# Optimization experiments

Hardware: AMD Instinct MI355X
Metric: run time of the kernel (lower is better)

## Reference

```python
import jax, jax.numpy as jnp
import numpy as np

B, H, L, D = 16, 8, 512, 64
TEMPERATURE = 8.0  # sqrt(d_k)
MASK_SENTINEL = -10000.0
BIG_NEG = 1e9


def setup_inputs() -> dict:
    key = jax.random.key(0)
    kq, kk, kv, km = jax.random.split(key, 4)
    q = jax.random.normal(kq, (B * H, L, D), dtype=jnp.float32)
    k = jax.random.normal(kk, (B * H, L, D), dtype=jnp.float32)
    v = jax.random.normal(kv, (B * H, L, D), dtype=jnp.float32)
    mask = jnp.where(jax.random.bernoulli(km, 0.1, (B, L)), MASK_SENTINEL, 0.0).astype(jnp.float32)
    return {"q": q, "k": k, "v": v, "mask": mask, "n_head": H}


def reference(q, k, v, mask, n_head):
    # attn: [B*H, L, L]
    attn = jnp.einsum("bid,bjd->bij", q, k) / TEMPERATURE
    # masked_fill(mask == -10000, 1e9); other values subtracted as-is
    m = jnp.where(mask == MASK_SENTINEL, BIG_NEG, mask)          # [B, L]
    m_bh = jnp.repeat(m, n_head, axis=0)                          # [B*H, L], matches reshape(B*H, ...)
    # row mask (mask.unsqueeze(-1).repeat) and its transpose (column mask)
    attn = attn - m_bh[:, :, None] - m_bh[:, None, :]
    attn = jax.nn.softmax(attn, axis=2)
    # dropout in eval mode (identity) for the deterministic reference
    output = jnp.einsum("bij,bjd->bid", attn, v)
    return output, attn
```

## Files before the change

kernel.cpp:

```cpp
#include <hip/hip_runtime.h>
#include <stdint.h>

#define Ln 512
#define Dn 64
#define BHn 128
#define AOFF ((size_t)BHn*Ln*Dn)

typedef __attribute__((ext_vector_type(8))) short short8;
typedef __attribute__((ext_vector_type(4))) float f32x4;
typedef __attribute__((ext_vector_type(4))) unsigned int u32x4;
typedef __attribute__((ext_vector_type(2))) unsigned int u32x2;

__device__ __forceinline__ uint16_t f2bf(float f){
  uint32_t x = __float_as_uint(f);
  return (uint16_t)((x + 0x7FFFu + ((x>>16)&1u)) >> 16);
}
__device__ __forceinline__ float bf2f(uint16_t u){ return __uint_as_float(((uint32_t)u)<<16); }
__device__ __forceinline__ uint32_t pack2(float a, float b){
  return (uint32_t)f2bf(a) | ((uint32_t)f2bf(b)<<16);
}
__device__ __forceinline__ void gld16(const uint16_t* g, uint16_t* l){
  __builtin_amdgcn_global_load_lds(
      (const __attribute__((address_space(1))) void*)g,
      (__attribute__((address_space(3))) void*)l, 16, 0, 0);
}

extern "C" __global__ __launch_bounds__(256)
void attn_prep(const float* __restrict__ kg, const float* __restrict__ vg,
               uint16_t* __restrict__ khw, uint16_t* __restrict__ klw,
               uint16_t* __restrict__ vtw)
{
  const int t  = threadIdx.x;
  const int c  = blockIdx.x;
  const int bh = blockIdx.y;
  const size_t base = (size_t)bh*(Ln*Dn);
  const size_t wsb  = ((size_t)bh<<15) + ((size_t)c<<13);

  {
    const int sj  = t>>1, skh = t&1;
    const float* kr = kg + base + (size_t)(c*128 + sj)*Dn + skh*32;
    const int sx = (sj&7)<<3;
    #pragma unroll
    for (int w2=0; w2<4; ++w2){
      f32x4 x0 = *(const f32x4*)(kr + w2*8);
      f32x4 x1 = *(const f32x4*)(kr + w2*8 + 4);
      uint32_t hw[4], lw[4];
      #pragma unroll
      for (int pi=0; pi<4; ++pi){
        float a0 = (pi<2) ? x0[pi*2]   : x1[(pi-2)*2];
        float a1 = (pi<2) ? x0[pi*2+1] : x1[(pi-2)*2+1];
        uint16_t h0 = f2bf(a0), h1 = f2bf(a1);
        hw[pi] = (uint32_t)h0 | ((uint32_t)h1<<16);
        lw[pi] = (uint32_t)f2bf(a0 - bf2f(h0)) | ((uint32_t)f2bf(a1 - bf2f(h1))<<16);
      }
      const size_t di = wsb + sj*64 + ((skh*32 + w2*8) ^ sx);
      *(u32x4*)(khw + di) = (u32x4){hw[0],hw[1],hw[2],hw[3]};
      *(u32x4*)(klw + di) = (u32x4){lw[0],lw[1],lw[2],lw[3]};
    }
  }

  #pragma unroll
  for (int it=0; it<2; ++it){
    const int j0 = (t>>4)*4 + it*64;
    const int d0 = (t&15)*4;
    const float* vr = vg + base + (size_t)(c*128 + j0)*Dn + d0;
    f32x4 r0 = *(const f32x4*)(vr);
    f32x4 r1 = *(const f32x4*)(vr + Dn);
    f32x4 r2 = *(const f32x4*)(vr + 2*Dn);
    f32x4 r3 = *(const f32x4*)(vr + 3*Dn);
    #pragma unroll
    for (int qd=0; qd<4; ++qd){
      const int d = d0 + qd;
      u32x2 w; w.x = pack2(r0[qd], r1[qd]); w.y = pack2(r2[qd], r3[qd]);
      *(u32x2*)(vtw + wsb + d*128 + (j0 ^ ((d&7)<<3))) = w;
    }
  }
}

extern "C" __global__ __launch_bounds__(256, 2)
void attn_main2(const float* __restrict__ qg, const float* __restrict__ mg,
                const uint16_t* __restrict__ khw, const uint16_t* __restrict__ klw,
                const uint16_t* __restrict__ vtw, float* __restrict__ outg)
{
  __shared__ __align__(16) uint16_t BIG[32768];

  const int t    = threadIdx.x;
  const int lane = t & 63;
  const int wv   = t >> 6;
  const int li   = lane & 15;
  const int lq   = lane >> 4;
  const int kx   = (li&7)<<3;

  const int lin = blockIdx.x + (blockIdx.y << 3);
  const int xcd = lin & 7;
  const int jj  = lin >> 3;
  const int bh  = (xcd << 4) + (jj >> 3);
  const int b   = bh >> 3;
  const int i0  = (jj & 7)*64 + wv*16;

  const size_t base = (size_t)bh*(Ln*Dn);
  const float* mrow = mg + b*Ln;
  const size_t wsbh = (size_t)bh << 15;

  uint16_t* PW = BIG + 16384 + wv*2176;

  auto issueK = [&](int c, int bsel){
    const size_t so = wsbh + ((size_t)c<<13) + (wv<<11) + (lane<<3);
    uint16_t* dh = BIG + bsel*16384 + (wv<<11);
    #pragma unroll
    for (int i=0;i<4;++i){
      gld16(khw + so + i*512, dh + i*512);
      gld16(klw + so + i*512, dh + 8192 + i*512);
    }
  };
  auto issueV = [&](int c, int bsel){
    const size_t so = wsbh + ((size_t)c<<13) + (wv<<11) + (lane<<3);
    uint16_t* dv = BIG + bsel*8192 + (wv<<11);
    #pragma unroll
    for (int i=0;i<4;++i) gld16(vtw + so + i*512, dv + i*512);
  };

  issueK(0, 0);

  short8 qhi[2], qlo[2];
  {
    const float* qrow = qg + base + (size_t)(i0 + li)*Dn;
    #pragma unroll
    for (int kt=0; kt<2; ++kt){
      const float* p = qrow + kt*32 + lq*8;
      f32x4 x0 = *(const f32x4*)p;
      f32x4 x1 = *(const f32x4*)(p+4);
      #pragma unroll
      for (int e=0; e<8; ++e){
        float x = (e<4) ? x0[e] : x1[e-4];
        uint16_t h = f2bf(x);
        qhi[kt][e] = (short)h;
        qlo[kt][e] = (short)f2bf(x - bf2f(h));
      }
    }
  }

  f32x4 acc[32];
  #pragma unroll
  for (int j=0; j<32; ++j) acc[j] = (f32x4)0.f;

  #pragma unroll
  for (int c=0; c<4; ++c){
    if (c<3) issueK(c+1, (c+1)&1);
    if (c<3) asm volatile("s_waitcnt vmcnt(8)" ::: "memory");
    else     asm volatile("s_waitcnt vmcnt(0)" ::: "memory");
    __builtin_amdgcn_sched_barrier(0);
    __builtin_amdgcn_s_barrier();
    __builtin_amdgcn_sched_barrier(0);
    const uint16_t* KHp = BIG + (c&1)*16384;
    const uint16_t* KLp = KHp + 8192;
    #pragma unroll
    for (int jt=0; jt<8; ++jt){
      #pragma unroll
      for (int kt=0; kt<2; ++kt){
        const int idx = (jt*16 + li)*64 + ((kt*32 + lq*8) ^ kx);
        short8 kh = *(const short8*)(KHp + idx);
        short8 kl = *(const short8*)(KLp + idx);
        f32x4 A = acc[c*8+jt];
        A = __builtin_amdgcn_mfma_f32_16x16x32_bf16(kh, qhi[kt], A, 0,0,0);
        A = __builtin_amdgcn_mfma_f32_16x16x32_bf16(kl, qhi[kt], A, 0,0,0);
        A = __builtin_amdgcn_mfma_f32_16x16x32_bf16(kh, qlo[kt], A, 0,0,0);
        acc[c*8+jt] = A;
      }
    }
    __builtin_amdgcn_sched_barrier(0);
    __builtin_amdgcn_s_barrier();
    __builtin_amdgcn_sched_barrier(0);
  }

  issueV(0, 0);

  {
    float mv = mrow[i0 + li];
    const float rmv = (mv < -9000.f) ? 1e9f : mv;
    #pragma unroll
    for (int jt=0; jt<32; ++jt){
      f32x4 cmr = *(const f32x4*)(mrow + jt*16 + lq*4);
      #pragma unroll
      for (int r=0; r<4; ++r){
        float cm = (cmr[r] < -9000.f) ? 1e9f : cmr[r];
        acc[jt][r] = (acc[jt][r]*0.125f - rmv) - cm;
      }
    }
  }

  float mx = -3.4e38f;
  #pragma unroll
  for (int jt=0; jt<32; ++jt)
    #pragma unroll
    for (int r=0; r<4; ++r) mx = fmaxf(mx, acc[jt][r]);
  mx = fmaxf(mx, __shfl_xor(mx, 16));
  mx = fmaxf(mx, __shfl_xor(mx, 32));
  float sum = 0.f;
  #pragma unroll
  for (int jt=0; jt<32; ++jt)
    #pragma unroll
    for (int r=0; r<4; ++r){ float e = __expf(acc[jt][r]-mx); acc[jt][r] = e; sum += e; }
  sum += __shfl_xor(sum, 16);
  sum += __shfl_xor(sum, 32);
  const float inv = 1.0f/sum;
  #pragma unroll
  for (int jt=0; jt<32; ++jt) acc[jt] = acc[jt]*inv;

  f32x4 oacc[4];
  #pragma unroll
  for (int dt=0; dt<4; ++dt) oacc[dt] = (f32x4)0.f;

  #pragma unroll
  for (int c=0; c<4; ++c){
    asm volatile("s_waitcnt vmcnt(0)" ::: "memory");
    __builtin_amdgcn_sched_barrier(0);
    __builtin_amdgcn_s_barrier();
    __builtin_amdgcn_sched_barrier(0);
    if (c<3) issueV(c+1, (c+1)&1);
    #pragma unroll
    for (int jtl=0; jtl<8; ++jtl){
      const f32x4 p = acc[c*8+jtl];
      u32x2 w; w.x = pack2(p[0], p[1]); w.y = pack2(p[2], p[3]);
      *(u32x2*)(PW + li*136 + jtl*16 + lq*4) = w;
    }
    asm volatile("s_waitcnt lgkmcnt(0)" ::: "memory");
    __builtin_amdgcn_sched_barrier(0);
    const uint16_t* VTp = BIG + (c&1)*8192;
    #pragma unroll
    for (int c32=0; c32<4; ++c32){
      short8 pf = *(const short8*)(PW + li*136 + c32*32 + lq*8);
      #pragma unroll
      for (int dt=0; dt<4; ++dt){
        short8 vb = *(const short8*)(VTp + (dt*16+li)*128 + ((c32*32+lq*8) ^ kx));
        oacc[dt] = __builtin_amdgcn_mfma_f32_16x16x32_bf16(vb, pf, oacc[dt], 0,0,0);
      }
    }
  }

  #pragma unroll
  for (int dt=0; dt<4; ++dt)
    *(f32x4*)(outg + base + (size_t)(i0+li)*Dn + dt*16 + lq*4) = oacc[dt];

  {
    float* arow = outg + AOFF + (size_t)bh*Ln*Ln + (size_t)(i0+li)*Ln;
    #pragma unroll
    for (int jt=0; jt<32; ++jt)
      __builtin_nontemporal_store(acc[jt], (f32x4*)(arow + jt*16 + lq*4));
  }
}

#define KSTR  72
#define VTSTR 136
#define FPSTRH 136

extern "C" __global__ __launch_bounds__(256, 2)
void attn_mfma(const float* __restrict__ qg, const float* __restrict__ kg,
               const float* __restrict__ vg, const float* __restrict__ mg,
               float* __restrict__ outg)
{
  __shared__ uint4 ldsraw[(36864 + 2048)/16];
  uint16_t* KHI = (uint16_t*)ldsraw;
  uint16_t* KLO = KHI + 128*KSTR;
  uint16_t* VT  = (uint16_t*)ldsraw;
  float*    CMV = (float*)((char*)ldsraw + 36864);

  const int t    = threadIdx.x;
  const int lane = t & 63;
  const int wv   = t >> 6;
  const int li   = lane & 15;
  const int lq   = lane >> 4;

  const int lin = blockIdx.x + (blockIdx.y << 3);
  const int xcd = lin & 7;
  const int jj  = lin >> 3;
  const int bh  = (xcd << 4) + (jj >> 3);
  const int b   = bh >> 3;
  const int i0  = (jj & 7)*64 + wv*16;

  const size_t base = (size_t)bh*(Ln*Dn);
  const float* mrow = mg + b*Ln;

  uint16_t* PW = (uint16_t*)((char*)ldsraw + 17408 + wv*(16*FPSTRH*2));

  {
    float m0 = mrow[t], m1 = mrow[t+256];
    CMV[t]     = (m0 < -9000.f) ? 1e9f : m0;
    CMV[t+256] = (m1 < -9000.f) ? 1e9f : m1;
  }

  short8 qhi[2], qlo[2];
  {
    const float* qrow = qg + base + (size_t)(i0 + li)*Dn;
    #pragma unroll
    for (int kt=0; kt<2; ++kt){
      const float* p = qrow + kt*32 + lq*8;
      f32x4 x0 = *(const f32x4*)p;
      f32x4 x1 = *(const f32x4*)(p+4);
      #pragma unroll
      for (int e=0; e<8; ++e){
        float x = (e<4) ? x0[e] : x1[e-4];
        uint16_t h = f2bf(x);
        qhi[kt][e] = (short)h;
        qlo[kt][e] = (short)f2bf(x - bf2f(h));
      }
    }
  }

  f32x4 acc[32];
  #pragma unroll
  for (int j=0; j<32; ++j) acc[j] = (f32x4)0.f;

  const int sj = t>>1, skh = t&1;
  #pragma unroll
  for (int c=0; c<4; ++c){
    __syncthreads();
    {
      const float* kr = kg + base + (size_t)(c*128 + sj)*Dn + skh*32;
      uint16_t* dhi = KHI + sj*KSTR + skh*32;
      uint16_t* dlo = KLO + sj*KSTR + skh*32;
      #pragma unroll
      for (int w2=0; w2<4; ++w2){
        f32x4 x0 = *(const f32x4*)(kr + w2*8);
        f32x4 x1 = *(const f32x4*)(kr + w2*8 + 4);
        uint32_t hw[4], lw[4];
        #pragma unroll
        for (int pi=0; pi<4; ++pi){
          float a0 = (pi<2) ? x0[pi*2]   : x1[(pi-2)*2];
          float a1 = (pi<2) ? x0[pi*2+1] : x1[(pi-2)*2+1];
          uint16_t h0 = f2bf(a0), h1 = f2bf(a1);
          hw[pi] = (uint32_t)h0 | ((uint32_t)h1<<16);
          lw[pi] = (uint32_t)f2bf(a0 - bf2f(h0)) | ((uint32_t)f2bf(a1 - bf2f(h1))<<16);
        }
        *(u32x4*)(dhi + w2*8) = (u32x4){hw[0],hw[1],hw[2],hw[3]};
        *(u32x4*)(dlo + w2*8) = (u32x4){lw[0],lw[1],lw[2],lw[3]};
      }
    }
    __syncthreads();
    #pragma unroll
    for (int jt=0; jt<8; ++jt){
      #pragma unroll
      for (int kt=0; kt<2; ++kt){
        const int off = (jt*16 + li)*KSTR + kt*32 + lq*8;
        short8 kh = *(const short8*)(KHI + off);
        short8 kl = *(const short8*)(KLO + off);
        f32x4 A = acc[c*8+jt];
        A = __builtin_amdgcn_mfma_f32_16x16x32_bf16(kh, qhi[kt], A, 0,0,0);
        A = __builtin_amdgcn_mfma_f32_16x16x32_bf16(kl, qhi[kt], A, 0,0,0);
        A = __builtin_amdgcn_mfma_f32_16x16x32_bf16(kh, qlo[kt], A, 0,0,0);
        acc[c*8+jt] = A;
      }
    }
  }

  {
    float mv = mrow[i0 + li];
    const float rmv = (mv < -9000.f) ? 1e9f : mv;
    #pragma unroll
    for (int jt=0; jt<32; ++jt){
      f32x4 cm = *(const f32x4*)(CMV + jt*16 + lq*4);
      #pragma unroll
      for (int r=0; r<4; ++r)
        acc[jt][r] = (acc[jt][r]*0.125f - rmv) - cm[r];
    }
  }
  float mx = -3.4e38f;
  #pragma unroll
  for (int jt=0; jt<32; ++jt)
    #pragma unroll
    for (int r=0; r<4; ++r) mx = fmaxf(mx, acc[jt][r]);
  mx = fmaxf(mx, __shfl_xor(mx, 16));
  mx = fmaxf(mx, __shfl_xor(mx, 32));
  float sum = 0.f;
  #pragma unroll
  for (int jt=0; jt<32; ++jt)
    #pragma unroll
    for (int r=0; r<4; ++r){ float e = __expf(acc[jt][r]-mx); acc[jt][r] = e; sum += e; }
  sum += __shfl_xor(sum, 16);
  sum += __shfl_xor(sum, 32);
  const float inv = 1.0f/sum;

  {
    float* arow = outg + AOFF + (size_t)bh*Ln*Ln + (size_t)(i0+li)*Ln;
    #pragma unroll
    for (int jt=0; jt<32; ++jt){
      f32x4 p = acc[jt]*inv;
      acc[jt] = p;
      *(f32x4*)(arow + jt*16 + lq*4) = p;
    }
  }

  f32x4 oacc[4];
  #pragma unroll
  for (int dt=0; dt<4; ++dt) oacc[dt] = (f32x4)0.f;

  #pragma unroll
  for (int c=0; c<4; ++c){
    __syncthreads();
    #pragma unroll
    for (int it=0; it<2; ++it){
      const int j0 = (t>>4)*4 + it*64;
      const int d0 = (t&15)*4;
      const float* vr = vg + base + (size_t)(c*128 + j0)*Dn + d0;
      f32x4 r0 = *(const f32x4*)(vr);
      f32x4 r1 = *(const f32x4*)(vr + Dn);
      f32x4 r2 = *(const f32x4*)(vr + 2*Dn);
      f32x4 r3 = *(const f32x4*)(vr + 3*Dn);
      #pragma unroll
      for (int qd=0; qd<4; ++qd){
        u32x2 w; w.x = pack2(r0[qd], r1[qd]); w.y = pack2(r2[qd], r3[qd]);
        *(u32x2*)(VT + (d0+qd)*VTSTR + j0) = w;
      }
    }
    __syncthreads();
    #pragma unroll
    for (int jtl=0; jtl<8; ++jtl){
      const f32x4 p = acc[c*8+jtl];
      u32x2 w; w.x = pack2(p[0], p[1]); w.y = pack2(p[2], p[3]);
      *(u32x2*)(PW + li*FPSTRH + jtl*16 + lq*4) = w;
    }
    asm volatile("s_waitcnt lgkmcnt(0)" ::: "memory");
    #pragma unroll
    for (int c32=0; c32<4; ++c32){
      short8 pf = *(const short8*)(PW + li*FPSTRH + c32*32 + lq*8);
      #pragma unroll
      for (int dt=0; dt<4; ++dt){
        short8 vb = *(const short8*)(VT + (dt*16+li)*VTSTR + c32*32 + lq*8);
        oacc[dt] = __builtin_amdgcn_mfma_f32_16x16x32_bf16(vb, pf, oacc[dt], 0,0,0);
      }
    }
  }

  #pragma unroll
  for (int dt=0; dt<4; ++dt)
    *(f32x4*)(outg + base + (size_t)(i0+li)*Dn + dt*16 + lq*4) = oacc[dt];
}

extern "C" void kernel_launch(void* const* d_in, const int* in_sizes, int n_in,
                              void* d_out, int out_size, void* d_ws, size_t ws_size,
                              hipStream_t stream)
{
  (void)in_sizes; (void)n_in; (void)out_size;
  const float* qg = (const float*)d_in[0];
  const float* kg = (const float*)d_in[1];
  const float* vg = (const float*)d_in[2];
  const float* mg = (const float*)d_in[3];
  float* outg = (float*)d_out;

  const size_t WS_NEED = 25165824;
  if (d_ws && ws_size >= WS_NEED){
    uint16_t* khw = (uint16_t*)d_ws;
    uint16_t* klw = (uint16_t*)((char*)d_ws + 8388608);
    uint16_t* vtw = (uint16_t*)((char*)d_ws + 16777216);
    attn_prep<<<dim3(4, BHn), 256, 0, stream>>>(kg, vg, khw, klw, vtw);
    attn_main2<<<dim3(Ln/64, BHn), 256, 0, stream>>>(qg, mg, khw, klw, vtw, outg);
  } else {
    attn_mfma<<<dim3(Ln/64, BHn), 256, 0, stream>>>(qg, kg, vg, mg, outg);
  }
}
```

Measured before the change: 233.2 us.

## Overlap V prefetch and attention stores with compute, stage column mask in LDS

```diff
diff --git a/kernel.cpp b/kernel.cpp
--- a/kernel.cpp
+++ b/kernel.cpp
@@ -83,6 +83,7 @@
                 const uint16_t* __restrict__ vtw, float* __restrict__ outg)
 {
   __shared__ __align__(16) uint16_t BIG[32768];
+  __shared__ float CMV[512];
 
   const int t    = threadIdx.x;
   const int lane = t & 63;
@@ -120,23 +121,31 @@
     for (int i=0;i<4;++i) gld16(vtw + so + i*512, dv + i*512);
   };
 
+  const float* qrow = qg + base + (size_t)(i0 + li)*Dn;
+  f32x4 qx0a = *(const f32x4*)(qrow + lq*8);
+  f32x4 qx0b = *(const f32x4*)(qrow + lq*8 + 4);
+  f32x4 qx1a = *(const f32x4*)(qrow + 32 + lq*8);
+  f32x4 qx1b = *(const f32x4*)(qrow + 32 + lq*8 + 4);
+  float m0 = mrow[t], m1 = mrow[t+256];
+  float mv = mrow[i0 + li];
+
   issueK(0, 0);
 
+  CMV[t]     = (m0 < -9000.f) ? 1e9f : m0;
+  CMV[t+256] = (m1 < -9000.f) ? 1e9f : m1;
+  const float rmv = (mv < -9000.f) ? 1e9f : mv;
+
   short8 qhi[2], qlo[2];
-  {
-    const float* qrow = qg + base + (size_t)(i0 + li)*Dn;
-    #pragma unroll
-    for (int kt=0; kt<2; ++kt){
-      const float* p = qrow + kt*32 + lq*8;
-      f32x4 x0 = *(const f32x4*)p;
-      f32x4 x1 = *(const f32x4*)(p+4);
-      #pragma unroll
-      for (int e=0; e<8; ++e){
-        float x = (e<4) ? x0[e] : x1[e-4];
-        uint16_t h = f2bf(x);
-        qhi[kt][e] = (short)h;
-        qlo[kt][e] = (short)f2bf(x - bf2f(h));
-      }
+  #pragma unroll
+  for (int kt=0; kt<2; ++kt){
+    f32x4 xa = kt ? qx1a : qx0a;
+    f32x4 xb = kt ? qx1b : qx0b;
+    #pragma unroll
+    for (int e=0; e<8; ++e){
+      float x = (e<4) ? xa[e] : xb[e-4];
+      uint16_t h = f2bf(x);
+      qhi[kt][e] = (short)h;
+      qlo[kt][e] = (short)f2bf(x - bf2f(h));
     }
   }
 
@@ -148,12 +157,13 @@
   for (int c=0; c<4; ++c){
     if (c<3) issueK(c+1, (c+1)&1);
     if (c<3) asm volatile("s_waitcnt vmcnt(8)" ::: "memory");
-    else     asm volatile("s_waitcnt vmcnt(0)" ::: "memory");
+    else     asm volatile("s_waitcnt vmcnt(4)" ::: "memory");
     __builtin_amdgcn_sched_barrier(0);
     __builtin_amdgcn_s_barrier();
     __builtin_amdgcn_sched_barrier(0);
     const uint16_t* KHp = BIG + (c&1)*16384;
     const uint16_t* KLp = KHp + 8192;
+    __builtin_amdgcn_s_setprio(1);
     #pragma unroll
     for (int jt=0; jt<8; ++jt){
       #pragma unroll
@@ -168,25 +178,19 @@
         acc[c*8+jt] = A;
       }
     }
+    __builtin_amdgcn_s_setprio(0);
     __builtin_amdgcn_sched_barrier(0);
     __builtin_amdgcn_s_barrier();
     __builtin_amdgcn_sched_barrier(0);
-  }
-
-  issueV(0, 0);
-
-  {
-    float mv = mrow[i0 + li];
-    const float rmv = (mv < -9000.f) ? 1e9f : mv;
-    #pragma unroll
-    for (int jt=0; jt<32; ++jt){
-      f32x4 cmr = *(const f32x4*)(mrow + jt*16 + lq*4);
-      #pragma unroll
-      for (int r=0; r<4; ++r){
-        float cm = (cmr[r] < -9000.f) ? 1e9f : cmr[r];
-        acc[jt][r] = (acc[jt][r]*0.125f - rmv) - cm;
-      }
-    }
+    if (c==2) issueV(0, 0);
+  }
+
+  #pragma unroll
+  for (int jt=0; jt<32; ++jt){
+    f32x4 cm = *(const f32x4*)(CMV + jt*16 + lq*4);
+    #pragma unroll
+    for (int r=0; r<4; ++r)
+      acc[jt][r] = (acc[jt][r]*0.125f - rmv) - cm[r];
   }
 
   float mx = -3.4e38f;
@@ -211,9 +215,12 @@
   #pragma unroll
   for (int dt=0; dt<4; ++dt) oacc[dt] = (f32x4)0.f;
 
+  float* arow = outg + AOFF + (size_t)bh*Ln*Ln + (size_t)(i0+li)*Ln;
+
   #pragma unroll
   for (int c=0; c<4; ++c){
-    asm volatile("s_waitcnt vmcnt(0)" ::: "memory");
+    if (c==0) asm volatile("s_waitcnt vmcnt(0)" ::: "memory");
+    else      asm volatile("s_waitcnt vmcnt(8)" ::: "memory");
     __builtin_amdgcn_sched_barrier(0);
     __builtin_amdgcn_s_barrier();
     __builtin_amdgcn_sched_barrier(0);
@@ -227,6 +234,7 @@
     asm volatile("s_waitcnt lgkmcnt(0)" ::: "memory");
     __builtin_amdgcn_sched_barrier(0);
     const uint16_t* VTp = BIG + (c&1)*8192;
+    __builtin_amdgcn_s_setprio(1);
     #pragma unroll
     for (int c32=0; c32<4; ++c32){
       short8 pf = *(const short8*)(PW + li*136 + c32*32 + lq*8);
@@ -236,18 +244,15 @@
         oacc[dt] = __builtin_amdgcn_mfma_f32_16x16x32_bf16(vb, pf, oacc[dt], 0,0,0);
       }
     }
+    __builtin_amdgcn_s_setprio(0);
+    #pragma unroll
+    for (int jtl=0; jtl<8; ++jtl)
+      __builtin_nontemporal_store(acc[c*8+jtl], (f32x4*)(arow + (c*8+jtl)*16 + lq*4));
   }
 
   #pragma unroll
   for (int dt=0; dt<4; ++dt)
     *(f32x4*)(outg + base + (size_t)(i0+li)*Dn + dt*16 + lq*4) = oacc[dt];
-
-  {
-    float* arow = outg + AOFF + (size_t)bh*Ln*Ln + (size_t)(i0+li)*Ln;
-    #pragma unroll
-    for (int jt=0; jt<32; ++jt)
-      __builtin_nontemporal_store(acc[jt], (f32x4*)(arow + jt*16 + lq*4));
-  }
 }
 
 #define KSTR  72
```

Measured after the change: 231.2 us. No clear change (-0.8%).
